# Kernel optimization log

Hardware: AMD Instinct MI355X
Metric: run time of the kernel (lower is better)

The kernel has to match this reference:

```python
import jax, jax.numpy as jnp
import numpy as np

NUM_JOINTS = 21
WINDOW = 131072  # window_size; pose3d has WINDOW+1 frames
N_BONES = NUM_JOINTS - 1
W_PROJ, W_BONE, W_SMOOTH, W_LIFT = 1.0, 1.0, 0.5, 0.1


def setup_inputs() -> dict:
    key = jax.random.key(0)
    k1, k2, k3, k4, k5 = jax.random.split(key, 5)
    pose3d = jax.random.normal(k1, (WINDOW + 1, 3, NUM_JOINTS), dtype=jnp.float32)
    camera_proj = jax.random.normal(k2, (WINDOW, 2, 3), dtype=jnp.float32)
    pose_2d = jax.random.normal(k3, (WINDOW, 2, NUM_JOINTS), dtype=jnp.float32)
    bone_lengths = jax.random.uniform(k4, (N_BONES,), dtype=jnp.float32)
    lift_directions = jax.random.normal(k5, (WINDOW, 3, N_BONES), dtype=jnp.float32)
    # normalize lift directions to unit vectors (they are bone directions)
    lift_directions = lift_directions / jnp.linalg.norm(lift_directions, axis=1, keepdims=True)
    # kinematic-chain bone connections: (child, parent) = (i+1, i), guaranteed distinct
    child = jnp.arange(1, NUM_JOINTS, dtype=jnp.int32)
    parent = jnp.arange(0, NUM_JOINTS - 1, dtype=jnp.int32)
    bone_connections = jnp.stack([child, parent], axis=1)  # [N_BONES, 2]
    lift_bone_connections = bone_connections
    return {
        "pose3d": pose3d,
        "camera_proj": camera_proj,
        "pose_2d": pose_2d,
        "bone_lengths": bone_lengths,
        "lift_directions": lift_directions,
        "bone_connections": bone_connections,
        "lift_bone_connections": lift_bone_connections,
    }


def reference(pose3d, camera_proj, pose_2d, bone_lengths, lift_directions,
              bone_connections, lift_bone_connections):
    J = NUM_JOINTS
    # --- projection loss: per-frame 2x3 camera applied to frames 1: ---
    projected = jnp.einsum('wij,wjk->wik', camera_proj, pose3d[1:])  # [W,2,J]
    proj_loss = jnp.sum(jnp.square(projected - pose_2d)) / (2 * J)
    # --- bone length loss ---
    d = pose3d[:, :, bone_connections[:, 0]] - pose3d[:, :, bone_connections[:, 1]]  # [W+1,3,NB]
    length_of_bone = jnp.sum(jnp.square(d), axis=1)  # [W+1, NB]
    bone_loss = jnp.sum(jnp.square(length_of_bone - bone_lengths[None, :])) / (J - 1)
    # --- smoothness loss (second difference) ---
    vel = pose3d[1:] - pose3d[:-1]  # [W,3,J]
    smooth_loss = jnp.sum(jnp.square(vel[1:] - vel[:-1])) / (3 * J)
    # --- lift direction loss ---
    bv = pose3d[1:, :, lift_bone_connections[:, 0]] - pose3d[1:, :, lift_bone_connections[:, 1]]  # [W,3,NB]
    norm = jnp.linalg.norm(bv, axis=1, keepdims=True)  # [W,1,NB]
    est_dirs = bv / norm
    lift_loss = jnp.sum(jnp.square(lift_directions - est_dirs)) / (3 * J)
    return (W_PROJ * proj_loss + W_BONE * bone_loss
            + W_SMOOTH * smooth_loss + W_LIFT * lift_loss)
```

## Files before the change

### kernel.cpp

```cpp
#include <hip/hip_runtime.h>
#include <math.h>

#define W 131072
#define NJ 21
#define NB 20
#define TILE 256
#define FR 63

__global__ void zero_kernel(float* out) { out[0] = 0.0f; }

__global__ __launch_bounds__(TILE) void pose3d_loss_kernel(
    const float* __restrict__ pose3d,
    const float* __restrict__ cam,
    const float* __restrict__ p2d,
    const float* __restrict__ blen,
    const float* __restrict__ ldir,
    const int* __restrict__ bcon,
    const int* __restrict__ lcon,
    float* __restrict__ out)
{
  __shared__ float sP[(TILE + 2) * FR];
  __shared__ float sBlen[NB];
  __shared__ int sBC[NB], sBP[NB], sLC[NB], sLP[NB];
  __shared__ float sWave[TILE / 64];

  const int tid = threadIdx.x;
  const int blk = blockIdx.x;
  const int f0 = blk * TILE;

  {
    const float* src = pose3d + (size_t)f0 * FR;
    const int limit = (W + 1) * FR - f0 * FR;
    const int total = (TILE + 2) * FR;
    for (int i = tid; i < total; i += TILE)
      sP[i] = (i < limit) ? src[i] : 0.0f;
  }
  if (tid < NB) {
    sBlen[tid] = blen[tid];
    sBC[tid] = bcon[2 * tid];
    sBP[tid] = bcon[2 * tid + 1];
    sLC[tid] = lcon[2 * tid];
    sLP[tid] = lcon[2 * tid + 1];
  }
  __syncthreads();

  const int w = f0 + tid;
  const float* P0 = sP + tid * FR;
  const float* P1 = P0 + FR;
  const float* P2 = P1 + FR;

  float p1f[FR];
#pragma unroll
  for (int i = 0; i < FR; ++i) p1f[i] = P1[i];

  float acc_proj = 0.f, acc_bone = 0.f, acc_smooth = 0.f, acc_lift = 0.f;

  {
    const float2* camv = (const float2*)(cam + (size_t)w * 6);
    float2 c0 = camv[0], c1 = camv[1], c2 = camv[2];
    float cr[2][3] = {{c0.x, c0.y, c1.x}, {c1.y, c2.x, c2.y}};
    const float2* pv = (const float2*)(p2d + (size_t)w * 42);
#pragma unroll
    for (int k = 0; k < 21; ++k) {
      float2 v = pv[k];
      {
        const int idx = 2 * k, i = idx / 21, j = idx % 21;
        float pr = cr[i][0] * p1f[j] + cr[i][1] * p1f[21 + j] + cr[i][2] * p1f[42 + j];
        float d = pr - v.x;
        acc_proj += d * d;
      }
      {
        const int idx = 2 * k + 1, i = idx / 21, j = idx % 21;
        float pr = cr[i][0] * p1f[j] + cr[i][1] * p1f[21 + j] + cr[i][2] * p1f[42 + j];
        float d = pr - v.y;
        acc_proj += d * d;
      }
    }
  }

  {
#pragma unroll
    for (int bb = 0; bb < NB; ++bb) {
      int ci = sBC[bb], pi = sBP[bb];
      float dx = P0[ci] - P0[pi];
      float dy = P0[21 + ci] - P0[21 + pi];
      float dz = P0[42 + ci] - P0[42 + pi];
      float L = dx * dx + dy * dy + dz * dz;
      float t = L - sBlen[bb];
      acc_bone += t * t;
    }
    if (w == W - 1) {
#pragma unroll
      for (int bb = 0; bb < NB; ++bb) {
        int ci = sBC[bb], pi = sBP[bb];
        float dx = P1[ci] - P1[pi];
        float dy = P1[21 + ci] - P1[21 + pi];
        float dz = P1[42 + ci] - P1[42 + pi];
        float L = dx * dx + dy * dy + dz * dz;
        float t = L - sBlen[bb];
        acc_bone += t * t;
      }
    }
  }

  if (w < W - 1) {
#pragma unroll
    for (int i = 0; i < FR; ++i) {
      float d2 = P2[i] - 2.0f * p1f[i] + P0[i];
      acc_smooth += d2 * d2;
    }
  }

  {
    const float4* lv = (const float4*)(ldir + (size_t)w * 60);
    float ld[60];
#pragma unroll
    for (int k = 0; k < 15; ++k) {
      float4 v = lv[k];
      ld[4 * k]     = v.x;
      ld[4 * k + 1] = v.y;
      ld[4 * k + 2] = v.z;
      ld[4 * k + 3] = v.w;
    }
#pragma unroll
    for (int bb = 0; bb < NB; ++bb) {
      int ci = sLC[bb], pi = sLP[bb];
      float bx = P1[ci] - P1[pi];
      float by = P1[21 + ci] - P1[21 + pi];
      float bz = P1[42 + ci] - P1[42 + pi];
      float inv = 1.0f / sqrtf(bx * bx + by * by + bz * bz);
      float ex = ld[bb]      - bx * inv;
      float ey = ld[20 + bb] - by * inv;
      float ez = ld[40 + bb] - bz * inv;
      acc_lift += ex * ex + ey * ey + ez * ez;
    }
  }

  float s = acc_proj * (1.0f / 42.0f) + acc_bone * (1.0f / 20.0f)
          + acc_smooth * (0.5f / 63.0f) + acc_lift * (0.1f / 63.0f);

#pragma unroll
  for (int off = 32; off > 0; off >>= 1) s += __shfl_down(s, off, 64);
  if ((tid & 63) == 0) sWave[tid >> 6] = s;
  __syncthreads();
  if (tid == 0) {
    float tot = 0.f;
#pragma unroll
    for (int i = 0; i < TILE / 64; ++i) tot += sWave[i];
    atomicAdd(out, tot);
  }
}

extern "C" void kernel_launch(void* const* d_in, const int* in_sizes, int n_in,
                              void* d_out, int out_size, void* d_ws, size_t ws_size,
                              hipStream_t stream) {
  const float* pose3d = (const float*)d_in[0];
  const float* cam    = (const float*)d_in[1];
  const float* p2d    = (const float*)d_in[2];
  const float* blen   = (const float*)d_in[3];
  const float* ldir   = (const float*)d_in[4];
  const int*   bcon   = (const int*)d_in[5];
  const int*   lcon   = (const int*)d_in[6];
  float* out = (float*)d_out;

  zero_kernel<<<1, 1, 0, stream>>>(out);
  pose3d_loss_kernel<<<W / TILE, TILE, 0, stream>>>(
      pose3d, cam, p2d, blen, ldir, bcon, lcon, out);
}
```

Measured before the change: 150.1 us.

## Map one wavefront per frame with lane-parallel losses and two-pass reduction

Replaces the thread-per-frame design, which staged tiles of frames in shared memory and kept large per-thread register arrays, with one 64-lane wavefront per frame. Each lane holds one pose coordinate, and cross-lane shuffles compute the projection, bone and lift terms. This gives coalesced per-frame loads and lower register pressure. The atomic accumulation and the zeroing kernel are replaced by per-block partial sums in the workspace plus a second reduction kernel. The cost is many more shuffle instructions and some idle lanes (64 lanes for 63 values, 42 or 60 active in some terms), and the workspace must hold 8192 floats.

```diff
diff --git a/kernel.cpp b/kernel.cpp
--- a/kernel.cpp
+++ b/kernel.cpp
@@ -2,14 +2,13 @@
 #include <math.h>
 
 #define W 131072
-#define NJ 21
+#define FR 63
 #define NB 20
-#define TILE 256
-#define FR 63
+#define WPB 16
+#define BLK (WPB * 64)
+#define NBLOCKS (W / WPB)
 
-__global__ void zero_kernel(float* out) { out[0] = 0.0f; }
-
-__global__ __launch_bounds__(TILE) void pose3d_loss_kernel(
+__global__ __launch_bounds__(BLK) void loss_pass1(
     const float* __restrict__ pose3d,
     const float* __restrict__ cam,
     const float* __restrict__ p2d,
@@ -17,137 +16,111 @@
     const float* __restrict__ ldir,
     const int* __restrict__ bcon,
     const int* __restrict__ lcon,
-    float* __restrict__ out)
+    float* __restrict__ partial)
 {
-  __shared__ float sP[(TILE + 2) * FR];
-  __shared__ float sBlen[NB];
-  __shared__ int sBC[NB], sBP[NB], sLC[NB], sLP[NB];
-  __shared__ float sWave[TILE / 64];
+  __shared__ float sWave[WPB];
+  const int tid  = threadIdx.x;
+  const int lane = tid & 63;
+  const int wv   = tid >> 6;
+  const int w    = blockIdx.x * WPB + wv;
+  const int wu   = __builtin_amdgcn_readfirstlane(w);
 
-  const int tid = threadIdx.x;
-  const int blk = blockIdx.x;
-  const int f0 = blk * TILE;
+  float P0 = 0.0f, P1 = 0.0f, P2 = 0.0f;
+  if (lane < FR) {
+    P0 = pose3d[(size_t)wu * FR + lane];
+    P1 = pose3d[(size_t)(wu + 1) * FR + lane];
+    if (wu < W - 1) P2 = pose3d[(size_t)(wu + 2) * FR + lane];
+  }
 
+  float d2 = P2 - 2.0f * P1 + P0;
+  float acc_smooth = (wu < W - 1) ? d2 * d2 : 0.0f;
+
+  float acc_proj = 0.0f;
   {
-    const float* src = pose3d + (size_t)f0 * FR;
-    const int limit = (W + 1) * FR - f0 * FR;
-    const int total = (TILE + 2) * FR;
-    for (int i = tid; i < total; i += TILE)
-      sP[i] = (i < limit) ? src[i] : 0.0f;
-  }
-  if (tid < NB) {
-    sBlen[tid] = blen[tid];
-    sBC[tid] = bcon[2 * tid];
-    sBP[tid] = bcon[2 * tid + 1];
-    sLC[tid] = lcon[2 * tid];
-    sLP[tid] = lcon[2 * tid + 1];
-  }
-  __syncthreads();
-
-  const int w = f0 + tid;
-  const float* P0 = sP + tid * FR;
-  const float* P1 = P0 + FR;
-  const float* P2 = P1 + FR;
-
-  float p1f[FR];
-#pragma unroll
-  for (int i = 0; i < FR; ++i) p1f[i] = P1[i];
-
-  float acc_proj = 0.f, acc_bone = 0.f, acc_smooth = 0.f, acc_lift = 0.f;
-
-  {
-    const float2* camv = (const float2*)(cam + (size_t)w * 6);
-    float2 c0 = camv[0], c1 = camv[1], c2 = camv[2];
-    float cr[2][3] = {{c0.x, c0.y, c1.x}, {c1.y, c2.x, c2.y}};
-    const float2* pv = (const float2*)(p2d + (size_t)w * 42);
-#pragma unroll
-    for (int k = 0; k < 21; ++k) {
-      float2 v = pv[k];
-      {
-        const int idx = 2 * k, i = idx / 21, j = idx % 21;
-        float pr = cr[i][0] * p1f[j] + cr[i][1] * p1f[21 + j] + cr[i][2] * p1f[42 + j];
-        float d = pr - v.x;
-        acc_proj += d * d;
-      }
-      {
-        const int idx = 2 * k + 1, i = idx / 21, j = idx % 21;
-        float pr = cr[i][0] * p1f[j] + cr[i][1] * p1f[21 + j] + cr[i][2] * p1f[42 + j];
-        float d = pr - v.y;
-        acc_proj += d * d;
-      }
+    int k = lane % 21;
+    float pk0 = __shfl(P1, k, 64);
+    float pk1 = __shfl(P1, k + 21, 64);
+    float pk2 = __shfl(P1, k + 42, 64);
+    const float* cp = cam + (size_t)wu * 6;
+    float c0 = cp[0], c1 = cp[1], c2 = cp[2], c3 = cp[3], c4 = cp[4], c5 = cp[5];
+    bool row1 = (lane >= 21);
+    float pr = row1 ? (c3 * pk0 + c4 * pk1 + c5 * pk2)
+                    : (c0 * pk0 + c1 * pk1 + c2 * pk2);
+    if (lane < 42) {
+      float t = p2d[(size_t)wu * 42 + lane];
+      float d = pr - t;
+      acc_proj = d * d;
     }
   }
 
+  int b = lane % 20;
+  int c = lane / 20; if (c > 2) c = 2;
+  const int2* bc2 = (const int2*)bcon;
+  const int2* lc2 = (const int2*)lcon;
+  int2 bcp = bc2[b];
+  int2 lcp = lc2[b];
+  float bl = blen[b];
+
+  float acc_bone = 0.0f;
   {
-#pragma unroll
-    for (int bb = 0; bb < NB; ++bb) {
-      int ci = sBC[bb], pi = sBP[bb];
-      float dx = P0[ci] - P0[pi];
-      float dy = P0[21 + ci] - P0[21 + pi];
-      float dz = P0[42 + ci] - P0[42 + pi];
-      float L = dx * dx + dy * dy + dz * dz;
-      float t = L - sBlen[bb];
-      acc_bone += t * t;
-    }
-    if (w == W - 1) {
-#pragma unroll
-      for (int bb = 0; bb < NB; ++bb) {
-        int ci = sBC[bb], pi = sBP[bb];
-        float dx = P1[ci] - P1[pi];
-        float dy = P1[21 + ci] - P1[21 + pi];
-        float dz = P1[42 + ci] - P1[42 + pi];
-        float L = dx * dx + dy * dy + dz * dz;
-        float t = L - sBlen[bb];
-        acc_bone += t * t;
-      }
+    int ic = c * 21 + bcp.x, ip = c * 21 + bcp.y;
+    float bx = __shfl(P1, ic, 64) - __shfl(P1, ip, 64);
+    float sq = bx * bx;
+    float L  = __shfl(sq, b, 64) + __shfl(sq, b + 20, 64) + __shfl(sq, b + 40, 64);
+    if (lane < 20) { float t = L - bl; acc_bone = t * t; }
+    if (wu == 0) {
+      float bx0 = __shfl(P0, ic, 64) - __shfl(P0, ip, 64);
+      float sq0 = bx0 * bx0;
+      float L0  = __shfl(sq0, b, 64) + __shfl(sq0, b + 20, 64) + __shfl(sq0, b + 40, 64);
+      if (lane < 20) { float t = L0 - bl; acc_bone += t * t; }
     }
   }
 
-  if (w < W - 1) {
-#pragma unroll
-    for (int i = 0; i < FR; ++i) {
-      float d2 = P2[i] - 2.0f * p1f[i] + P0[i];
-      acc_smooth += d2 * d2;
+  float acc_lift = 0.0f;
+  {
+    int ic = c * 21 + lcp.x, ip = c * 21 + lcp.y;
+    float lx  = __shfl(P1, ic, 64) - __shfl(P1, ip, 64);
+    float lsq = lx * lx;
+    float LL  = __shfl(lsq, b, 64) + __shfl(lsq, b + 20, 64) + __shfl(lsq, b + 40, 64);
+    if (lane < 60) {
+      float inv = rsqrtf(LL);
+      float est = lx * inv;
+      float ld  = ldir[(size_t)wu * 60 + lane];
+      float d   = ld - est;
+      acc_lift = d * d;
     }
   }
 
-  {
-    const float4* lv = (const float4*)(ldir + (size_t)w * 60);
-    float ld[60];
+  float total = acc_proj * (1.0f / 42.0f) + acc_bone * (1.0f / 20.0f)
+              + acc_smooth * (0.5f / 63.0f) + acc_lift * (0.1f / 63.0f);
 #pragma unroll
-    for (int k = 0; k < 15; ++k) {
-      float4 v = lv[k];
-      ld[4 * k]     = v.x;
-      ld[4 * k + 1] = v.y;
-      ld[4 * k + 2] = v.z;
-      ld[4 * k + 3] = v.w;
-    }
-#pragma unroll
-    for (int bb = 0; bb < NB; ++bb) {
-      int ci = sLC[bb], pi = sLP[bb];
-      float bx = P1[ci] - P1[pi];
-      float by = P1[21 + ci] - P1[21 + pi];
-      float bz = P1[42 + ci] - P1[42 + pi];
-      float inv = 1.0f / sqrtf(bx * bx + by * by + bz * bz);
-      float ex = ld[bb]      - bx * inv;
-      float ey = ld[20 + bb] - by * inv;
-      float ez = ld[40 + bb] - bz * inv;
-      acc_lift += ex * ex + ey * ey + ez * ez;
-    }
-  }
-
-  float s = acc_proj * (1.0f / 42.0f) + acc_bone * (1.0f / 20.0f)
-          + acc_smooth * (0.5f / 63.0f) + acc_lift * (0.1f / 63.0f);
-
-#pragma unroll
-  for (int off = 32; off > 0; off >>= 1) s += __shfl_down(s, off, 64);
-  if ((tid & 63) == 0) sWave[tid >> 6] = s;
+  for (int off = 32; off > 0; off >>= 1) total += __shfl_xor(total, off, 64);
+  if (lane == 0) sWave[wv] = total;
   __syncthreads();
   if (tid == 0) {
-    float tot = 0.f;
+    float s = 0.0f;
 #pragma unroll
-    for (int i = 0; i < TILE / 64; ++i) tot += sWave[i];
-    atomicAdd(out, tot);
+    for (int i = 0; i < WPB; ++i) s += sWave[i];
+    partial[blockIdx.x] = s;
+  }
+}
+
+__global__ __launch_bounds__(1024) void loss_pass2(
+    const float* __restrict__ partial, float* __restrict__ out)
+{
+  __shared__ float sW[16];
+  int tid = threadIdx.x;
+  float s = 0.0f;
+  for (int i = tid; i < NBLOCKS; i += 1024) s += partial[i];
+#pragma unroll
+  for (int off = 32; off > 0; off >>= 1) s += __shfl_xor(s, off, 64);
+  if ((tid & 63) == 0) sW[tid >> 6] = s;
+  __syncthreads();
+  if (tid == 0) {
+    float t = 0.0f;
+#pragma unroll
+    for (int i = 0; i < 16; ++i) t += sW[i];
+    out[0] = t;
   }
 }
 
@@ -161,9 +134,10 @@
   const float* ldir   = (const float*)d_in[4];
   const int*   bcon   = (const int*)d_in[5];
   const int*   lcon   = (const int*)d_in[6];
-  float* out = (float*)d_out;
+  float* out     = (float*)d_out;
+  float* partial = (float*)d_ws;
 
-  zero_kernel<<<1, 1, 0, stream>>>(out);
-  pose3d_loss_kernel<<<W / TILE, TILE, 0, stream>>>(
-      pose3d, cam, p2d, blen, ldir, bcon, lcon, out);
+  loss_pass1<<<NBLOCKS, BLK, 0, stream>>>(pose3d, cam, p2d, blen, ldir,
+                                          bcon, lcon, partial);
+  loss_pass2<<<1, 1024, 0, stream>>>(partial, out);
 }
```

New measurement: 156.5 us. 4.3% more time.

## Use 64-frame blocks with padded LDS, vectorized loads, and two-pass reduction

Applied to the files above, without the earlier changes.

Shrinks blocks to 64 frames, with a padded shared-memory pitch of 67 to avoid bank conflicts. The pose tile is loaded with float4 reads. The bone-length and lift-direction loops share one squared-length computation when the connections match, and rsqrt replaces 1/sqrt. Per-block partials go to workspace and a second single-block kernel sums them, which removes the zero kernel and the atomics. The cost is a higher halo overhead (66/64 instead of 258/256 frames) and a slightly less accurate rsqrt.

```diff
diff --git a/kernel.cpp b/kernel.cpp
--- a/kernel.cpp
+++ b/kernel.cpp
@@ -2,14 +2,14 @@
 #include <math.h>
 
 #define W 131072
-#define NJ 21
+#define FR 63
 #define NB 20
-#define TILE 256
-#define FR 63
+#define BLKT 64
+#define TFR (BLKT + 2)
+#define PITCH 67
+#define NBLOCKS (W / BLKT)
 
-__global__ void zero_kernel(float* out) { out[0] = 0.0f; }
-
-__global__ __launch_bounds__(TILE) void pose3d_loss_kernel(
+__global__ __launch_bounds__(BLKT) void loss_pass1(
     const float* __restrict__ pose3d,
     const float* __restrict__ cam,
     const float* __restrict__ p2d,
@@ -17,44 +17,59 @@
     const float* __restrict__ ldir,
     const int* __restrict__ bcon,
     const int* __restrict__ lcon,
-    float* __restrict__ out)
+    float* __restrict__ partial)
 {
-  __shared__ float sP[(TILE + 2) * FR];
-  __shared__ float sBlen[NB];
-  __shared__ int sBC[NB], sBP[NB], sLC[NB], sLP[NB];
-  __shared__ float sWave[TILE / 64];
-
+  __shared__ float sP[TFR * PITCH];
   const int tid = threadIdx.x;
   const int blk = blockIdx.x;
-  const int f0 = blk * TILE;
+  const int f0 = blk * BLKT;
+  const int w  = f0 + tid;
 
   {
     const float* src = pose3d + (size_t)f0 * FR;
-    const int limit = (W + 1) * FR - f0 * FR;
-    const int total = (TILE + 2) * FR;
-    for (int i = tid; i < total; i += TILE)
-      sP[i] = (i < limit) ? src[i] : 0.0f;
-  }
-  if (tid < NB) {
-    sBlen[tid] = blen[tid];
-    sBC[tid] = bcon[2 * tid];
-    sBP[tid] = bcon[2 * tid + 1];
-    sLC[tid] = lcon[2 * tid];
-    sLP[tid] = lcon[2 * tid + 1];
+    const int avail = (W + 1) * FR - f0 * FR;
+    const int lim = (TFR * FR < avail) ? TFR * FR : avail;
+    const int n4 = (TFR * FR + 3) / 4;
+    for (int q = tid; q < n4; q += BLKT) {
+      int j = 4 * q;
+      int f = j / FR, e = j - f * FR;
+      if (j + 3 < lim) {
+        float4 v = *(const float4*)(src + j);
+        float vv[4] = {v.x, v.y, v.z, v.w};
+#pragma unroll
+        for (int k = 0; k < 4; ++k) {
+          sP[f * PITCH + e] = vv[k];
+          if (++e == FR) { e = 0; ++f; }
+        }
+      } else {
+#pragma unroll
+        for (int k = 0; k < 4; ++k) {
+          if (j + k < lim) sP[f * PITCH + e] = src[j + k];
+          if (++e == FR) { e = 0; ++f; }
+        }
+      }
+    }
   }
   __syncthreads();
 
-  const int w = f0 + tid;
-  const float* P0 = sP + tid * FR;
-  const float* P1 = P0 + FR;
-  const float* P2 = P1 + FR;
+  const float* P0 = sP + tid * PITCH;
+  const float* P1 = P0 + PITCH;
+  const float* P2 = P1 + PITCH;
 
-  float p1f[FR];
+  float p1[FR];
 #pragma unroll
-  for (int i = 0; i < FR; ++i) p1f[i] = P1[i];
+  for (int e = 0; e < FR; ++e) p1[e] = P1[e];
 
-  float acc_proj = 0.f, acc_bone = 0.f, acc_smooth = 0.f, acc_lift = 0.f;
+  float acc_smooth = 0.0f;
+  if (w < W - 1) {
+#pragma unroll
+    for (int e = 0; e < FR; ++e) {
+      float d2 = P2[e] - 2.0f * p1[e] + P0[e];
+      acc_smooth += d2 * d2;
+    }
+  }
 
+  float acc_proj = 0.0f;
   {
     const float2* camv = (const float2*)(cam + (size_t)w * 6);
     float2 c0 = camv[0], c1 = camv[1], c2 = camv[2];
@@ -65,89 +80,94 @@
       float2 v = pv[k];
       {
         const int idx = 2 * k, i = idx / 21, j = idx % 21;
-        float pr = cr[i][0] * p1f[j] + cr[i][1] * p1f[21 + j] + cr[i][2] * p1f[42 + j];
+        float pr = cr[i][0] * p1[j] + cr[i][1] * p1[21 + j] + cr[i][2] * p1[42 + j];
         float d = pr - v.x;
         acc_proj += d * d;
       }
       {
         const int idx = 2 * k + 1, i = idx / 21, j = idx % 21;
-        float pr = cr[i][0] * p1f[j] + cr[i][1] * p1f[21 + j] + cr[i][2] * p1f[42 + j];
+        float pr = cr[i][0] * p1[j] + cr[i][1] * p1[21 + j] + cr[i][2] * p1[42 + j];
         float d = pr - v.y;
         acc_proj += d * d;
       }
     }
   }
 
+  float acc_bone = 0.0f, acc_lift = 0.0f;
   {
+    const int2* bc2 = (const int2*)bcon;
+    const int2* lc2 = (const int2*)lcon;
+    const float4* lv = (const float4*)(ldir + (size_t)w * 60);
+    float ld[60];
 #pragma unroll
-    for (int bb = 0; bb < NB; ++bb) {
-      int ci = sBC[bb], pi = sBP[bb];
-      float dx = P0[ci] - P0[pi];
-      float dy = P0[21 + ci] - P0[21 + pi];
-      float dz = P0[42 + ci] - P0[42 + pi];
-      float L = dx * dx + dy * dy + dz * dz;
-      float t = L - sBlen[bb];
+    for (int k = 0; k < 15; ++k) {
+      float4 v = lv[k];
+      ld[4 * k] = v.x; ld[4 * k + 1] = v.y; ld[4 * k + 2] = v.z; ld[4 * k + 3] = v.w;
+    }
+#pragma unroll
+    for (int b = 0; b < NB; ++b) {
+      int2 lc = lc2[b];
+      float dx = P1[lc.x]      - P1[lc.y];
+      float dy = P1[21 + lc.x] - P1[21 + lc.y];
+      float dz = P1[42 + lc.x] - P1[42 + lc.y];
+      float S  = dx * dx + dy * dy + dz * dz;
+      float inv = rsqrtf(S);
+      float ex = ld[b]      - dx * inv;
+      float ey = ld[20 + b] - dy * inv;
+      float ez = ld[40 + b] - dz * inv;
+      acc_lift += ex * ex + ey * ey + ez * ez;
+
+      int2 bc = bc2[b];
+      float Sb;
+      if (bc.x == lc.x && bc.y == lc.y) {
+        Sb = S;
+      } else {
+        float bx = P1[bc.x]      - P1[bc.y];
+        float by = P1[21 + bc.x] - P1[21 + bc.y];
+        float bz = P1[42 + bc.x] - P1[42 + bc.y];
+        Sb = bx * bx + by * by + bz * bz;
+      }
+      float t = Sb - blen[b];
       acc_bone += t * t;
     }
-    if (w == W - 1) {
+    if (w == 0) {
 #pragma unroll
-      for (int bb = 0; bb < NB; ++bb) {
-        int ci = sBC[bb], pi = sBP[bb];
-        float dx = P1[ci] - P1[pi];
-        float dy = P1[21 + ci] - P1[21 + pi];
-        float dz = P1[42 + ci] - P1[42 + pi];
-        float L = dx * dx + dy * dy + dz * dz;
-        float t = L - sBlen[bb];
+      for (int b = 0; b < NB; ++b) {
+        int2 bc = bc2[b];
+        float bx = P0[bc.x]      - P0[bc.y];
+        float by = P0[21 + bc.x] - P0[21 + bc.y];
+        float bz = P0[42 + bc.x] - P0[42 + bc.y];
+        float Sb = bx * bx + by * by + bz * bz;
+        float t = Sb - blen[b];
         acc_bone += t * t;
       }
     }
   }
 
-  if (w < W - 1) {
-#pragma unroll
-    for (int i = 0; i < FR; ++i) {
-      float d2 = P2[i] - 2.0f * p1f[i] + P0[i];
-      acc_smooth += d2 * d2;
-    }
-  }
-
-  {
-    const float4* lv = (const float4*)(ldir + (size_t)w * 60);
-    float ld[60];
-#pragma unroll
-    for (int k = 0; k < 15; ++k) {
-      float4 v = lv[k];
-      ld[4 * k]     = v.x;
-      ld[4 * k + 1] = v.y;
-      ld[4 * k + 2] = v.z;
-      ld[4 * k + 3] = v.w;
-    }
-#pragma unroll
-    for (int bb = 0; bb < NB; ++bb) {
-      int ci = sLC[bb], pi = sLP[bb];
-      float bx = P1[ci] - P1[pi];
-      float by = P1[21 + ci] - P1[21 + pi];
-      float bz = P1[42 + ci] - P1[42 + pi];
-      float inv = 1.0f / sqrtf(bx * bx + by * by + bz * bz);
-      float ex = ld[bb]      - bx * inv;
-      float ey = ld[20 + bb] - by * inv;
-      float ez = ld[40 + bb] - bz * inv;
-      acc_lift += ex * ex + ey * ey + ez * ez;
-    }
-  }
-
   float s = acc_proj * (1.0f / 42.0f) + acc_bone * (1.0f / 20.0f)
           + acc_smooth * (0.5f / 63.0f) + acc_lift * (0.1f / 63.0f);
+#pragma unroll
+  for (int off = 32; off > 0; off >>= 1) s += __shfl_xor(s, off, 64);
+  if (tid == 0) partial[blk] = s;
+}
 
+__global__ __launch_bounds__(256) void loss_pass2(
+    const float* __restrict__ partial, float* __restrict__ out)
+{
+  __shared__ float sW[4];
+  int tid = threadIdx.x;
+  float s = 0.0f;
 #pragma unroll
-  for (int off = 32; off > 0; off >>= 1) s += __shfl_down(s, off, 64);
-  if ((tid & 63) == 0) sWave[tid >> 6] = s;
+  for (int i = 0; i < NBLOCKS / 256; ++i) s += partial[i * 256 + tid];
+#pragma unroll
+  for (int off = 32; off > 0; off >>= 1) s += __shfl_xor(s, off, 64);
+  if ((tid & 63) == 0) sW[tid >> 6] = s;
   __syncthreads();
   if (tid == 0) {
-    float tot = 0.f;
+    float t = 0.0f;
 #pragma unroll
-    for (int i = 0; i < TILE / 64; ++i) tot += sWave[i];
-    atomicAdd(out, tot);
+    for (int i = 0; i < 4; ++i) t += sW[i];
+    out[0] = t;
   }
 }
 
@@ -161,9 +181,10 @@
   const float* ldir   = (const float*)d_in[4];
   const int*   bcon   = (const int*)d_in[5];
   const int*   lcon   = (const int*)d_in[6];
-  float* out = (float*)d_out;
+  float* out     = (float*)d_out;
+  float* partial = (float*)d_ws;
 
-  zero_kernel<<<1, 1, 0, stream>>>(out);
-  pose3d_loss_kernel<<<W / TILE, TILE, 0, stream>>>(
-      pose3d, cam, p2d, blen, ldir, bcon, lcon, out);
+  loss_pass1<<<NBLOCKS, BLKT, 0, stream>>>(pose3d, cam, p2d, blen, ldir,
+                                           bcon, lcon, partial);
+  loss_pass2<<<1, 256, 0, stream>>>(partial, out);
 }
```

Measured after the change: 138.3 us. 1.08x faster.
